# Performance work log

Measured on AMD Instinct MI355X. Metric: run time of the kernel, lower is better.

The kernel has to match this reference:

```python
import jax, jax.numpy as jnp
import numpy as np

N_NODES = 100000
N_EDGES = 1600000
NUM_GRAPHS = 128


def _gcn_layer(x, W, b, senders, receivers, n_node):
    # Linear transform first (cheaper: feature dim small)
    x = x @ W + b  # [N, out]
    ones = jnp.ones(senders.shape[0], dtype=x.dtype)
    deg_s = jax.ops.segment_sum(ones, senders, n_node)     # out-degree
    deg_r = jax.ops.segment_sum(ones, receivers, n_node)   # in-degree
    # symmetric normalization: D^-1/2 A D^-1/2
    x = x * jax.lax.rsqrt(jnp.maximum(deg_s, 1.0))[:, None]
    x = jax.ops.segment_sum(x[senders], receivers, n_node)  # gather-scatter aggregation
    x = x * jax.lax.rsqrt(jnp.maximum(deg_r, 1.0))[:, None]
    return x


def setup_inputs() -> dict:
    key = jax.random.key(0)
    ks = jax.random.split(key, 10)
    x = jax.random.normal(ks[0], (N_NODES, 9), dtype=jnp.float32)
    senders = jax.random.randint(ks[1], (N_EDGES,), 0, N_NODES)
    receivers = jax.random.randint(ks[2], (N_EDGES,), 0, N_NODES)
    batch = jnp.sort(jax.random.randint(ks[3], (N_NODES,), 0, NUM_GRAPHS))
    # learned params (Dense: W [in,out], b [out]) with LeCun-normal-ish scale
    def dense(k, din, dout):
        return jax.random.normal(k, (din, dout), dtype=jnp.float32) / np.sqrt(din)
    W1 = dense(ks[4], 9, 64)
    b1 = jnp.zeros((64,), jnp.float32)
    W2 = dense(ks[5], 64, 128)
    b2 = jnp.zeros((128,), jnp.float32)
    W3 = dense(ks[6], 128, 2)
    b3 = jnp.zeros((2,), jnp.float32)
    return {"x": x, "senders": senders, "receivers": receivers, "batch": batch,
            "num_graphs": NUM_GRAPHS, "W1": W1, "b1": b1, "W2": W2, "b2": b2,
            "W3": W3, "b3": b3}


def reference(x, senders, receivers, batch, num_graphs, W1, b1, W2, b2, W3, b3):
    n_node = x.shape[0]
    x = jax.nn.relu(_gcn_layer(x, W1, b1, senders, receivers, n_node))
    x = jax.nn.relu(_gcn_layer(x, W2, b2, senders, receivers, n_node))
    x = _gcn_layer(x, W3, b3, senders, receivers, n_node)
    # graph-level pooling
    return jax.ops.segment_sum(x, batch, num_graphs)
```

## Files before the change

### kernel.cpp

```cpp
#include <hip/hip_runtime.h>
#include <hip/hip_bf16.h>
#include <cstddef>

#define NBMAX 512
#define BCAP 5120
#define BKCHUNK 3200

typedef unsigned short bf16t;
typedef __attribute__((ext_vector_type(8))) short short8;
typedef __attribute__((ext_vector_type(4))) float f32x4;

static __device__ __forceinline__ float2 up2(unsigned u) {
    return make_float2(__uint_as_float(u << 16), __uint_as_float(u & 0xffff0000u));
}
static __device__ __forceinline__ bf16t f2bf(float f) {
    unsigned u = __float_as_uint(f);
    u += 0x7fffu + ((u >> 16) & 1u);
    return (bf16t)(u >> 16);
}
static __device__ __forceinline__ unsigned pk2(float a, float b) {
    return (unsigned)f2bf(a) | ((unsigned)f2bf(b) << 16);
}

__global__ void k_bucket(const int* __restrict__ S, const int* __restrict__ R,
                         unsigned* __restrict__ bufR, unsigned char* __restrict__ bufS,
                         int* __restrict__ gCntR, int* __restrict__ gCntS,
                         const float* __restrict__ W2, bf16t* __restrict__ W2f,
                         int nE, int nB) {
    __shared__ int histR[NBMAX], lstR[NBMAX], baseR[NBMAX];
    __shared__ int histS[NBMAX], lstS[NBMAX], baseS[NBMAX];
    __shared__ int sm[256];
    __shared__ unsigned sortedR[BKCHUNK];
    __shared__ unsigned short bOfR[BKCHUNK];
    __shared__ unsigned char sortedS[BKCHUNK];
    __shared__ unsigned short bOfS[BKCHUNK];
    int t = threadIdx.x;
    int nSort = gridDim.x - 4;
    if (blockIdx.x >= nSort) {
        int tt = (blockIdx.x - nSort) * blockDim.x + t;
        if (tt < 1024) {
            int nt = tt >> 7, kh = (tt >> 6) & 1, lane = tt & 63;
            int n = nt * 16 + (lane & 15);
            int k0 = kh * 32 + (lane >> 4) * 8;
            uint4 p;
            p.x = pk2(W2[(k0 + 0) * 128 + n], W2[(k0 + 1) * 128 + n]);
            p.y = pk2(W2[(k0 + 2) * 128 + n], W2[(k0 + 3) * 128 + n]);
            p.z = pk2(W2[(k0 + 4) * 128 + n], W2[(k0 + 5) * 128 + n]);
            p.w = pk2(W2[(k0 + 6) * 128 + n], W2[(k0 + 7) * 128 + n]);
            ((uint4*)W2f)[tt] = p;
        }
        return;
    }
    for (int i = t; i < NBMAX; i += 256) { histR[i] = 0; histS[i] = 0; }
    __syncthreads();
    int chunk = (nE + nSort - 1) / nSort;
    int e0 = blockIdx.x * chunk;
    int e1 = min(e0 + chunk, nE);
    for (int e = e0 + t; e < e1; e += 256) {
        atomicAdd(&histR[R[e] >> 8], 1);
        atomicAdd(&histS[S[e] >> 8], 1);
    }
    __syncthreads();
    {
        int c0 = histR[2 * t], c1 = histR[2 * t + 1];
        int ps = c0 + c1;
        sm[t] = ps;
        __syncthreads();
        for (int off = 1; off < 256; off <<= 1) {
            int y = (t >= off) ? sm[t - off] : 0;
            __syncthreads();
            sm[t] += y;
            __syncthreads();
        }
        int ex = sm[t] - ps;
        lstR[2 * t] = ex;
        lstR[2 * t + 1] = ex + c0;
    }
    __syncthreads();
    {
        int c0 = histS[2 * t], c1 = histS[2 * t + 1];
        int ps = c0 + c1;
        sm[t] = ps;
        __syncthreads();
        for (int off = 1; off < 256; off <<= 1) {
            int y = (t >= off) ? sm[t - off] : 0;
            __syncthreads();
            sm[t] += y;
            __syncthreads();
        }
        int ex = sm[t] - ps;
        lstS[2 * t] = ex;
        lstS[2 * t + 1] = ex + c0;
    }
    __syncthreads();
    for (int i = t; i < nB; i += 256) {
        int cR = histR[i];
        baseR[i] = cR ? atomicAdd(&gCntR[i], cR) : 0;
        int cS = histS[i];
        baseS[i] = cS ? atomicAdd(&gCntS[i], cS) : 0;
    }
    for (int i = t; i < NBMAX; i += 256) { histR[i] = 0; histS[i] = 0; }
    __syncthreads();
    for (int e = e0 + t; e < e1; e += 256) {
        int r = R[e], s = S[e];
        int br = r >> 8;
        int p = lstR[br] + atomicAdd(&histR[br], 1);
        sortedR[p] = ((unsigned)(r & 255) << 24) | (unsigned)s;
        bOfR[p] = (unsigned short)br;
        int bs = s >> 8;
        int p2 = lstS[bs] + atomicAdd(&histS[bs], 1);
        sortedS[p2] = (unsigned char)(s & 255);
        bOfS[p2] = (unsigned short)bs;
    }
    __syncthreads();
    int cnt = e1 - e0;
    for (int i = t; i < cnt; i += 256) {
        int b = bOfR[i];
        int slot = baseR[b] + (i - lstR[b]);
        if (slot < BCAP) bufR[(size_t)b * BCAP + slot] = sortedR[i];
        int b2 = bOfS[i];
        int slot2 = baseS[b2] + (i - lstS[b2]);
        if (slot2 < BCAP) bufS[(size_t)b2 * BCAP + slot2] = sortedS[i];
    }
}

__global__ void k_pass2(const unsigned* __restrict__ bufR, const unsigned char* __restrict__ bufS,
                        const int* __restrict__ gCntR, const int* __restrict__ gCntS,
                        const float* __restrict__ x,
                        int* __restrict__ csr, int* __restrict__ cur, int* __restrict__ degR,
                        float* __restrict__ inv_r, float* __restrict__ inv_s,
                        bf16t* __restrict__ xs, int nN, int nB) {
    __shared__ int hist[256], incl[256], curs[256], histS[256];
    __shared__ int sm[256];
    __shared__ int gex[NBMAX];
    int t = threadIdx.x;
    int b = blockIdx.x;
    {
        int c0 = (2 * t < nB) ? gCntR[2 * t] : 0;
        int c1 = (2 * t + 1 < nB) ? gCntR[2 * t + 1] : 0;
        int ps = c0 + c1;
        sm[t] = ps;
        __syncthreads();
        for (int off = 1; off < 256; off <<= 1) {
            int y = (t >= off) ? sm[t - off] : 0;
            __syncthreads();
            sm[t] += y;
            __syncthreads();
        }
        int ex = sm[t] - ps;
        gex[2 * t] = ex;
        gex[2 * t + 1] = ex + c0;
    }
    hist[t] = 0; curs[t] = 0; histS[t] = 0;
    __syncthreads();
    int gb = gex[b];
    int cnt = gCntR[b];
    const unsigned* buf = bufR + (size_t)b * BCAP;
    for (int i = t; i < cnt; i += 256) atomicAdd(&hist[buf[i] >> 24], 1);
    __syncthreads();
    int v = hist[t];
    sm[t] = v;
    __syncthreads();
    for (int off = 1; off < 256; off <<= 1) {
        int y = (t >= off) ? sm[t - off] : 0;
        __syncthreads();
        sm[t] += y;
        __syncthreads();
    }
    incl[t] = sm[t];
    __syncthreads();
    int n0 = b << 8;
    int n = n0 + t;
    if (n < nN) {
        degR[n] = v;
        cur[n] = gb + incl[t];
        inv_r[n] = rsqrtf(fmaxf((float)v, 1.f));
    }
    for (int i = t; i < cnt; i += 256) {
        unsigned p = buf[i];
        int rl = p >> 24;
        int s = p & 0xFFFFFF;
        int pos = gb + (incl[rl] - hist[rl]) + atomicAdd(&curs[rl], 1);
        csr[pos] = s;
    }
    int cntS = gCntS[b];
    const unsigned char* bufs = bufS + (size_t)b * BCAP;
    for (int i = t; i < cntS; i += 256) atomicAdd(&histS[bufs[i]], 1);
    __syncthreads();
    if (n < nN) {
        float is = rsqrtf(fmaxf((float)histS[t], 1.f));
        inv_s[n] = is;
        float w[9];
#pragma unroll
        for (int k = 0; k < 9; k++) w[k] = x[(size_t)n * 9 + k] * is;
        uint4 pa, pb;
        pa.x = pk2(w[0], w[1]); pa.y = pk2(w[2], w[3]);
        pa.z = pk2(w[4], w[5]); pa.w = pk2(w[6], w[7]);
        pb.x = pk2(w[8], is);   pb.y = 0; pb.z = 0; pb.w = 0;
        uint4* o = (uint4*)(xs + (size_t)n * 16);
        o[0] = pa;
        o[1] = pb;
    }
}

__global__ void k_h1f(const unsigned* __restrict__ xs32, const float* __restrict__ W1,
                      const float* __restrict__ b1,
                      const int* __restrict__ csr, const int* __restrict__ cur,
                      const int* __restrict__ degR, const float* __restrict__ inv_r,
                      const float* __restrict__ inv_s,
                      bf16t* __restrict__ h1s, float* __restrict__ warr, int nN) {
    __shared__ float Wl[9 * 64];
    __shared__ float bl[64];
    for (int i = threadIdx.x; i < 9 * 64; i += blockDim.x) Wl[i] = W1[i];
    if (threadIdx.x < 64) bl[threadIdx.x] = b1[threadIdx.x];
    __syncthreads();
    int lane = threadIdx.x & 63;
    int wave = threadIdx.x >> 6;
    int n = blockIdx.x * 16 + wave * 4 + (lane >> 4);
    int ql = lane & 15;
    int g = ql >> 2;
    int f2 = ql & 3;
    int nc = min(n, nN - 1);
    int deg = degR[nc];
    int st = cur[nc] - deg;
    float4 A0 = {0.f, 0.f, 0.f, 0.f}, A1 = A0, A2 = A0, A3 = A0;
    int i = 0;
    for (; i + 16 <= deg; i += 16) {
        int ea = csr[st + i + g];
        int eb = csr[st + i + 4 + g];
        int ec = csr[st + i + 8 + g];
        int ed = csr[st + i + 12 + g];
        uint2 u0 = *(const uint2*)(xs32 + (size_t)ea * 8 + f2 * 2);
        uint2 u1 = *(const uint2*)(xs32 + (size_t)eb * 8 + f2 * 2);
        uint2 u2 = *(const uint2*)(xs32 + (size_t)ec * 8 + f2 * 2);
        uint2 u3 = *(const uint2*)(xs32 + (size_t)ed * 8 + f2 * 2);
        float2 a = up2(u0.x), b = up2(u0.y);
        A0.x += a.x; A0.y += a.y; A0.z += b.x; A0.w += b.y;
        a = up2(u1.x); b = up2(u1.y);
        A1.x += a.x; A1.y += a.y; A1.z += b.x; A1.w += b.y;
        a = up2(u2.x); b = up2(u2.y);
        A2.x += a.x; A2.y += a.y; A2.z += b.x; A2.w += b.y;
        a = up2(u3.x); b = up2(u3.y);
        A3.x += a.x; A3.y += a.y; A3.z += b.x; A3.w += b.y;
    }
    for (; i + 4 <= deg; i += 4) {
        int ea = csr[st + i + g];
        uint2 u0 = *(const uint2*)(xs32 + (size_t)ea * 8 + f2 * 2);
        float2 a = up2(u0.x), b = up2(u0.y);
        A0.x += a.x; A0.y += a.y; A0.z += b.x; A0.w += b.y;
    }
    if (g < deg - i) {
        int ea = csr[st + i + g];
        uint2 u0 = *(const uint2*)(xs32 + (size_t)ea * 8 + f2 * 2);
        float2 a = up2(u0.x), b = up2(u0.y);
        A1.x += a.x; A1.y += a.y; A1.z += b.x; A1.w += b.y;
    }
    float4 vq = {(A0.x + A1.x) + (A2.x + A3.x), (A0.y + A1.y) + (A2.y + A3.y),
                 (A0.z + A1.z) + (A2.z + A3.z), (A0.w + A1.w) + (A2.w + A3.w)};
    vq.x += __shfl_xor(vq.x, 4); vq.y += __shfl_xor(vq.y, 4);
    vq.z += __shfl_xor(vq.z, 4); vq.w += __shfl_xor(vq.w, 4);
    vq.x += __shfl_xor(vq.x, 8); vq.y += __shfl_xor(vq.y, 8);
    vq.z += __shfl_xor(vq.z, 8); vq.w += __shfl_xor(vq.w, 8);
    int base = lane & 48;
    float xv[9];
    xv[0] = __shfl(vq.x, base + 0); xv[1] = __shfl(vq.y, base + 0);
    xv[2] = __shfl(vq.z, base + 0); xv[3] = __shfl(vq.w, base + 0);
    xv[4] = __shfl(vq.x, base + 1); xv[5] = __shfl(vq.y, base + 1);
    xv[6] = __shfl(vq.z, base + 1); xv[7] = __shfl(vq.w, base + 1);
    xv[8] = __shfl(vq.x, base + 2);
    float w = __shfl(vq.y, base + 2);
    float ir = inv_r[nc];
    float is = inv_s[nc];
    int c0 = ql * 4;
    float acc[4];
#pragma unroll
    for (int j = 0; j < 4; j++) acc[j] = w * bl[c0 + j];
#pragma unroll
    for (int k = 0; k < 9; k++) {
        float4 wv = *(const float4*)(Wl + k * 64 + c0);
        acc[0] += xv[k] * wv.x;
        acc[1] += xv[k] * wv.y;
        acc[2] += xv[k] * wv.z;
        acc[3] += xv[k] * wv.w;
    }
    if (n < nN) {
        float v0 = fmaxf(acc[0] * ir, 0.f) * is;
        float v1 = fmaxf(acc[1] * ir, 0.f) * is;
        float v2 = fmaxf(acc[2] * ir, 0.f) * is;
        float v3 = fmaxf(acc[3] * ir, 0.f) * is;
        uint2 pv;
        pv.x = pk2(v0, v1);
        pv.y = pk2(v2, v3);
        *(uint2*)(h1s + (size_t)n * 64 + c0) = pv;
        if (ql == 0) warr[n] = w;
    }
}

__global__ void __launch_bounds__(128, 6)
k_l2f(const unsigned* __restrict__ h32, const bf16t* __restrict__ W2f,
      const float* __restrict__ b2, const float* __restrict__ W3,
      const float* __restrict__ inv_r, const float* __restrict__ inv_s,
      const float* __restrict__ warr,
      const int* __restrict__ csr, const int* __restrict__ cur,
      const int* __restrict__ degR,
      float* __restrict__ t, float* __restrict__ dout, int outSize, int nN) {
    __shared__ float b2l[128];
    __shared__ float W3l[256];
    __shared__ unsigned zl[32 * 36];
    for (int i = threadIdx.x; i < 128; i += blockDim.x) b2l[i] = b2[i];
    for (int i = threadIdx.x; i < 256; i += blockDim.x) W3l[i] = W3[i];
    if (blockIdx.x == 0)
        for (int i = threadIdx.x; i < outSize; i += blockDim.x) dout[i] = 0.f;
    int lane = threadIdx.x & 63;
    int wave = threadIdx.x >> 6;
    int qw = lane >> 4;
    int ql = lane & 15;
    int n0w = blockIdx.x * 32 + wave * 16;
    for (int j2 = 0; j2 < 4; j2++) {
        int roff = qw * 4 + j2;
        int nc = min(n0w + roff, nN - 1);
        int deg = degR[nc];
        int st = cur[nc] - deg;
        float4 A0 = {0.f, 0.f, 0.f, 0.f}, A1 = A0, A2 = A0, A3 = A0;
        int i = 0;
        for (; i + 8 <= deg; i += 8) {
            int e0 = csr[st + i + 0];
            int e1 = csr[st + i + 1];
            int e2 = csr[st + i + 2];
            int e3 = csr[st + i + 3];
            int e4 = csr[st + i + 4];
            int e5 = csr[st + i + 5];
            int e6 = csr[st + i + 6];
            int e7 = csr[st + i + 7];
            uint2 u0 = *(const uint2*)(h32 + (size_t)e0 * 32 + ql * 2);
            uint2 u1 = *(const uint2*)(h32 + (size_t)e1 * 32 + ql * 2);
            uint2 u2 = *(const uint2*)(h32 + (size_t)e2 * 32 + ql * 2);
            uint2 u3 = *(const uint2*)(h32 + (size_t)e3 * 32 + ql * 2);
            uint2 u4 = *(const uint2*)(h32 + (size_t)e4 * 32 + ql * 2);
            uint2 u5 = *(const uint2*)(h32 + (size_t)e5 * 32 + ql * 2);
            uint2 u6 = *(const uint2*)(h32 + (size_t)e6 * 32 + ql * 2);
            uint2 u7 = *(const uint2*)(h32 + (size_t)e7 * 32 + ql * 2);
            float2 a = up2(u0.x), bb = up2(u0.y);
            A0.x += a.x; A0.y += a.y; A0.z += bb.x; A0.w += bb.y;
            a = up2(u1.x); bb = up2(u1.y);
            A1.x += a.x; A1.y += a.y; A1.z += bb.x; A1.w += bb.y;
            a = up2(u2.x); bb = up2(u2.y);
            A2.x += a.x; A2.y += a.y; A2.z += bb.x; A2.w += bb.y;
            a = up2(u3.x); bb = up2(u3.y);
            A3.x += a.x; A3.y += a.y; A3.z += bb.x; A3.w += bb.y;
            a = up2(u4.x); bb = up2(u4.y);
            A0.x += a.x; A0.y += a.y; A0.z += bb.x; A0.w += bb.y;
            a = up2(u5.x); bb = up2(u5.y);
            A1.x += a.x; A1.y += a.y; A1.z += bb.x; A1.w += bb.y;
            a = up2(u6.x); bb = up2(u6.y);
            A2.x += a.x; A2.y += a.y; A2.z += bb.x; A2.w += bb.y;
            a = up2(u7.x); bb = up2(u7.y);
            A3.x += a.x; A3.y += a.y; A3.z += bb.x; A3.w += bb.y;
        }
        if (i + 4 <= deg) {
            int e0 = csr[st + i + 0];
            int e1 = csr[st + i + 1];
            int e2 = csr[st + i + 2];
            int e3 = csr[st + i + 3];
            uint2 u0 = *(const uint2*)(h32 + (size_t)e0 * 32 + ql * 2);
            uint2 u1 = *(const uint2*)(h32 + (size_t)e1 * 32 + ql * 2);
            uint2 u2 = *(const uint2*)(h32 + (size_t)e2 * 32 + ql * 2);
            uint2 u3 = *(const uint2*)(h32 + (size_t)e3 * 32 + ql * 2);
            float2 a = up2(u0.x), bb = up2(u0.y);
            A0.x += a.x; A0.y += a.y; A0.z += bb.x; A0.w += bb.y;
            a = up2(u1.x); bb = up2(u1.y);
            A1.x += a.x; A1.y += a.y; A1.z += bb.x; A1.w += bb.y;
            a = up2(u2.x); bb = up2(u2.y);
            A2.x += a.x; A2.y += a.y; A2.z += bb.x; A2.w += bb.y;
            a = up2(u3.x); bb = up2(u3.y);
            A3.x += a.x; A3.y += a.y; A3.z += bb.x; A3.w += bb.y;
            i += 4;
        }
        if (i < deg) {
            int ea = csr[st + i];
            uint2 u0 = *(const uint2*)(h32 + (size_t)ea * 32 + ql * 2);
            float2 a = up2(u0.x), bb = up2(u0.y);
            A0.x += a.x; A0.y += a.y; A0.z += bb.x; A0.w += bb.y;
            i++;
        }
        if (i < deg) {
            int ea = csr[st + i];
            uint2 u0 = *(const uint2*)(h32 + (size_t)ea * 32 + ql * 2);
            float2 a = up2(u0.x), bb = up2(u0.y);
            A1.x += a.x; A1.y += a.y; A1.z += bb.x; A1.w += bb.y;
            i++;
        }
        if (i < deg) {
            int ea = csr[st + i];
            uint2 u0 = *(const uint2*)(h32 + (size_t)ea * 32 + ql * 2);
            float2 a = up2(u0.x), bb = up2(u0.y);
            A2.x += a.x; A2.y += a.y; A2.z += bb.x; A2.w += bb.y;
        }
        float4 v = {(A0.x + A1.x) + (A2.x + A3.x), (A0.y + A1.y) + (A2.y + A3.y),
                    (A0.z + A1.z) + (A2.z + A3.z), (A0.w + A1.w) + (A2.w + A3.w)};
        uint2 pv;
        pv.x = pk2(v.x, v.y);
        pv.y = pk2(v.z, v.w);
        *(uint2*)(zl + (wave * 16 + roff) * 36 + ql * 2) = pv;
    }
    __syncthreads();
    int m = ql;
    int q = lane >> 4;
    int row = wave * 16 + m;
    short8 afr0 = *(const short8*)(zl + row * 36 + q * 4);
    short8 afr1 = *(const short8*)(zl + row * 36 + 16 + q * 4);
    float w4[4], ir4[4], is4[4];
#pragma unroll
    for (int reg = 0; reg < 4; reg++) {
        int nr = min(n0w + q * 4 + reg, nN - 1);
        w4[reg] = warr[nr];
        ir4[reg] = inv_r[nr];
        is4[reg] = inv_s[nr];
    }
    float p0[4] = {0.f, 0.f, 0.f, 0.f}, p1[4] = {0.f, 0.f, 0.f, 0.f};
#pragma unroll
    for (int nt = 0; nt < 8; nt++) {
        short8 b0 = *(const short8*)(W2f + ((size_t)(nt * 2 + 0) * 64 + lane) * 8);
        short8 b1 = *(const short8*)(W2f + ((size_t)(nt * 2 + 1) * 64 + lane) * 8);
        f32x4 acc = {0.f, 0.f, 0.f, 0.f};
        acc = __builtin_amdgcn_mfma_f32_16x16x32_bf16(afr0, b0, acc, 0, 0, 0);
        acc = __builtin_amdgcn_mfma_f32_16x16x32_bf16(afr1, b1, acc, 0, 0, 0);
        int col = nt * 16 + m;
        float bc = b2l[col];
        float w30 = W3l[col * 2 + 0];
        float w31 = W3l[col * 2 + 1];
#pragma unroll
        for (int reg = 0; reg < 4; reg++) {
            float h = fmaxf((acc[reg] + w4[reg] * bc) * ir4[reg], 0.f) * is4[reg];
            p0[reg] += h * w30;
            p1[reg] += h * w31;
        }
    }
#pragma unroll
    for (int mask = 1; mask < 16; mask <<= 1) {
#pragma unroll
        for (int reg = 0; reg < 4; reg++) {
            p0[reg] += __shfl_xor(p0[reg], mask);
            p1[reg] += __shfl_xor(p1[reg], mask);
        }
    }
    if (m == 0) {
#pragma unroll
        for (int reg = 0; reg < 4; reg++) {
            int nr = n0w + q * 4 + reg;
            if (nr < nN) *(float2*)(t + (size_t)nr * 2) = make_float2(p0[reg], p1[reg]);
        }
    }
}

__global__ void k_poolg(const float* __restrict__ t, const float* __restrict__ inv_r,
                        const float* __restrict__ warr, const float* __restrict__ b3,
                        const int* __restrict__ csr, const int* __restrict__ cur,
                        const int* __restrict__ degR, const int* __restrict__ batch,
                        float* out, int nN, int outSize) {
    __shared__ float sm[256];
    for (int i = threadIdx.x; i < 256; i += blockDim.x) sm[i] = 0.f;
    __syncthreads();
    int tid = blockIdx.x * blockDim.x + threadIdx.x;
    int n = tid >> 2;
    int sub = tid & 3;
    if (n < nN) {
        int deg = degR[n];
        int st = cur[n] - deg;
        float a0 = 0.f, a1 = 0.f, c0 = 0.f, c1 = 0.f;
        float d0 = 0.f, d1 = 0.f, e0 = 0.f, e1 = 0.f;
        int i = sub;
        for (; i + 12 < deg; i += 16) {
            int sa = csr[st + i], sb = csr[st + i + 4];
            int sc = csr[st + i + 8], sd = csr[st + i + 12];
            float2 va = ((const float2*)t)[sa];
            float2 vb = ((const float2*)t)[sb];
            float2 vc = ((const float2*)t)[sc];
            float2 vd = ((const float2*)t)[sd];
            a0 += va.x; a1 += va.y;
            c0 += vb.x; c1 += vb.y;
            d0 += vc.x; d1 += vc.y;
            e0 += vd.x; e1 += vd.y;
        }
        for (; i < deg; i += 4) {
            float2 va = ((const float2*)t)[csr[st + i]];
            a0 += va.x; a1 += va.y;
        }
        float p0 = (a0 + c0) + (d0 + e0);
        float p1 = (a1 + c1) + (d1 + e1);
        p0 += __shfl_xor(p0, 1); p1 += __shfl_xor(p1, 1);
        p0 += __shfl_xor(p0, 2); p1 += __shfl_xor(p1, 2);
        if (sub == 0) {
            float ir = inv_r[n];
            float wb = warr[n] * ir;
            int g = batch[n];
            atomicAdd(&sm[2 * g + 0], p0 * ir + wb * b3[0]);
            atomicAdd(&sm[2 * g + 1], p1 * ir + wb * b3[1]);
        }
    }
    __syncthreads();
    for (int i = threadIdx.x; i < outSize; i += blockDim.x) {
        float v = sm[i];
        if (v != 0.f) atomicAdd(&out[i], v);
    }
}

extern "C" void kernel_launch(void* const* d_in, const int* in_sizes, int n_in,
                              void* d_out, int out_size, void* d_ws, size_t ws_size,
                              hipStream_t stream) {
    const float* x     = (const float*)d_in[0];
    const int*   S     = (const int*)d_in[1];
    const int*   R     = (const int*)d_in[2];
    const int*   batch = (const int*)d_in[3];
    const float* W1 = (const float*)d_in[5];
    const float* b1 = (const float*)d_in[6];
    const float* W2 = (const float*)d_in[7];
    const float* b2 = (const float*)d_in[8];
    const float* W3 = (const float*)d_in[9];
    const float* b3 = (const float*)d_in[10];

    int nN = in_sizes[0] / 9;
    int nE = in_sizes[1];
    int nB = (nN + 255) / 256;

    char* ws = (char*)d_ws;
    int*   cur   = (int*)ws;
    int*   degR  = cur + nN;
    float* inv_s = (float*)(degR + nN);
    float* inv_r = inv_s + nN;
    float* warr  = inv_r + nN;
    int*   gCntR = (int*)(warr + nN);
    int*   gCntS = gCntR + NBMAX;
    int*   csr   = gCntS + NBMAX;
    bf16t* xs    = (bf16t*)(csr + nE);
    bf16t* W2f   = xs + (size_t)nN * 16;
    char*  regA  = (char*)(W2f + 8192);
    unsigned*      bufR = (unsigned*)regA;
    unsigned char* bufS = (unsigned char*)(bufR + (size_t)NBMAX * BCAP);
    bf16t* h1s = (bf16t*)regA;
    float* t   = (float*)(regA + (size_t)NBMAX * BCAP * 5);

    const int B = 256;

    hipMemsetAsync(gCntR, 0, 2 * NBMAX * 4, stream);
    k_bucket<<<516, B, 0, stream>>>(S, R, bufR, bufS, gCntR, gCntS, W2, W2f, nE, nB);
    k_pass2<<<nB, B, 0, stream>>>(bufR, bufS, gCntR, gCntS, x, csr, cur, degR,
                                  inv_r, inv_s, xs, nN, nB);

    k_h1f<<<(nN + 15) / 16, B, 0, stream>>>((const unsigned*)xs, W1, b1, csr, cur, degR,
                                            inv_r, inv_s, h1s, warr, nN);

    k_l2f<<<(nN + 31) / 32, 128, 0, stream>>>((const unsigned*)h1s, W2f, b2, W3,
                                              inv_r, inv_s, warr, csr, cur, degR,
                                              t, (float*)d_out, out_size, nN);

    k_poolg<<<(nN * 4 + B - 1) / B, B, 0, stream>>>(t, inv_r, warr, b3, csr, cur, degR, batch,
                                                    (float*)d_out, nN, out_size);
}
```

Baseline: 221.3 us.

## Halve rows per block in layer-2 fused kernel and widen pool gather to 8 lanes

The layer-2 fused kernel now handles 16 nodes per 128-thread block, with both waves splitting the gather (2 rows per quarter-wave instead of 4). Both waves then compute the same MFMA tile and only wave 0 writes the result. Launch bounds rise to 8 blocks per SIMD. The pooling kernel uses 8 lanes per node instead of 4. The goal is more parallelism on the latency-bound edge gathers, at the cost of duplicated MFMA work and more blocks.

```diff
diff --git a/kernel.cpp b/kernel.cpp
--- a/kernel.cpp
+++ b/kernel.cpp
@@ -296,7 +296,7 @@
     }
 }
 
-__global__ void __launch_bounds__(128, 6)
+__global__ void __launch_bounds__(128, 8)
 k_l2f(const unsigned* __restrict__ h32, const bf16t* __restrict__ W2f,
       const float* __restrict__ b2, const float* __restrict__ W3,
       const float* __restrict__ inv_r, const float* __restrict__ inv_s,
@@ -306,7 +306,7 @@
       float* __restrict__ t, float* __restrict__ dout, int outSize, int nN) {
     __shared__ float b2l[128];
     __shared__ float W3l[256];
-    __shared__ unsigned zl[32 * 36];
+    __shared__ unsigned zl[16 * 36];
     for (int i = threadIdx.x; i < 128; i += blockDim.x) b2l[i] = b2[i];
     for (int i = threadIdx.x; i < 256; i += blockDim.x) W3l[i] = W3[i];
     if (blockIdx.x == 0)
@@ -315,10 +315,10 @@
     int wave = threadIdx.x >> 6;
     int qw = lane >> 4;
     int ql = lane & 15;
-    int n0w = blockIdx.x * 32 + wave * 16;
-    for (int j2 = 0; j2 < 4; j2++) {
-        int roff = qw * 4 + j2;
-        int nc = min(n0w + roff, nN - 1);
+    int n0b = blockIdx.x * 16;
+    for (int j2 = 0; j2 < 2; j2++) {
+        int roff = wave * 8 + qw * 2 + j2;
+        int nc = min(n0b + roff, nN - 1);
         int deg = degR[nc];
         int st = cur[nc] - deg;
         float4 A0 = {0.f, 0.f, 0.f, 0.f}, A1 = A0, A2 = A0, A3 = A0;
@@ -401,18 +401,17 @@
         uint2 pv;
         pv.x = pk2(v.x, v.y);
         pv.y = pk2(v.z, v.w);
-        *(uint2*)(zl + (wave * 16 + roff) * 36 + ql * 2) = pv;
+        *(uint2*)(zl + roff * 36 + ql * 2) = pv;
     }
     __syncthreads();
     int m = ql;
-    int q = lane >> 4;
-    int row = wave * 16 + m;
-    short8 afr0 = *(const short8*)(zl + row * 36 + q * 4);
-    short8 afr1 = *(const short8*)(zl + row * 36 + 16 + q * 4);
+    int q = qw;
+    short8 afr0 = *(const short8*)(zl + m * 36 + q * 4);
+    short8 afr1 = *(const short8*)(zl + m * 36 + 16 + q * 4);
     float w4[4], ir4[4], is4[4];
 #pragma unroll
     for (int reg = 0; reg < 4; reg++) {
-        int nr = min(n0w + q * 4 + reg, nN - 1);
+        int nr = min(n0b + q * 4 + reg, nN - 1);
         w4[reg] = warr[nr];
         ir4[reg] = inv_r[nr];
         is4[reg] = inv_s[nr];
@@ -444,10 +443,10 @@
             p1[reg] += __shfl_xor(p1[reg], mask);
         }
     }
-    if (m == 0) {
+    if (wave == 0 && m == 0) {
 #pragma unroll
         for (int reg = 0; reg < 4; reg++) {
-            int nr = n0w + q * 4 + reg;
+            int nr = n0b + q * 4 + reg;
             if (nr < nN) *(float2*)(t + (size_t)nr * 2) = make_float2(p0[reg], p1[reg]);
         }
     }
@@ -462,34 +461,29 @@
     for (int i = threadIdx.x; i < 256; i += blockDim.x) sm[i] = 0.f;
     __syncthreads();
     int tid = blockIdx.x * blockDim.x + threadIdx.x;
-    int n = tid >> 2;
-    int sub = tid & 3;
+    int n = tid >> 3;
+    int sub = tid & 7;
     if (n < nN) {
         int deg = degR[n];
         int st = cur[n] - deg;
         float a0 = 0.f, a1 = 0.f, c0 = 0.f, c1 = 0.f;
-        float d0 = 0.f, d1 = 0.f, e0 = 0.f, e1 = 0.f;
         int i = sub;
-        for (; i + 12 < deg; i += 16) {
-            int sa = csr[st + i], sb = csr[st + i + 4];
-            int sc = csr[st + i + 8], sd = csr[st + i + 12];
+        for (; i + 8 < deg; i += 16) {
+            int sa = csr[st + i], sb = csr[st + i + 8];
             float2 va = ((const float2*)t)[sa];
             float2 vb = ((const float2*)t)[sb];
-            float2 vc = ((const float2*)t)[sc];
-            float2 vd = ((const float2*)t)[sd];
             a0 += va.x; a1 += va.y;
             c0 += vb.x; c1 += vb.y;
-            d0 += vc.x; d1 += vc.y;
-            e0 += vd.x; e1 += vd.y;
-        }
-        for (; i < deg; i += 4) {
+        }
+        for (; i < deg; i += 8) {
             float2 va = ((const float2*)t)[csr[st + i]];
             a0 += va.x; a1 += va.y;
         }
-        float p0 = (a0 + c0) + (d0 + e0);
-        float p1 = (a1 + c1) + (d1 + e1);
+        float p0 = a0 + c0;
+        float p1 = a1 + c1;
         p0 += __shfl_xor(p0, 1); p1 += __shfl_xor(p1, 1);
         p0 += __shfl_xor(p0, 2); p1 += __shfl_xor(p1, 2);
+        p0 += __shfl_xor(p0, 4); p1 += __shfl_xor(p1, 4);
         if (sub == 0) {
             float ir = inv_r[n];
             float wb = warr[n] * ir;
@@ -550,10 +544,10 @@
     k_h1f<<<(nN + 15) / 16, B, 0, stream>>>((const unsigned*)xs, W1, b1, csr, cur, degR,
                                             inv_r, inv_s, h1s, warr, nN);
 
-    k_l2f<<<(nN + 31) / 32, 128, 0, stream>>>((const unsigned*)h1s, W2f, b2, W3,
+    k_l2f<<<(nN + 15) / 16, 128, 0, stream>>>((const unsigned*)h1s, W2f, b2, W3,
                                               inv_r, inv_s, warr, csr, cur, degR,
                                               t, (float*)d_out, out_size, nN);
 
-    k_poolg<<<(nN * 4 + B - 1) / B, B, 0, stream>>>(t, inv_r, warr, b3, csr, cur, degR, batch,
+    k_poolg<<<(nN * 8 + B - 1) / B, B, 0, stream>>>(t, inv_r, warr, b3, csr, cur, degR, batch,
                                                     (float*)d_out, nN, out_size);
 }
```

New measurement: 223.8 us. No clear change (+1.1%).
